# Kernel optimization log

Hardware: AMD Instinct MI355X
Metric: run time of the kernel (lower is better)

## Reference

```python
import jax, jax.numpy as jnp
import numpy as np

NS, NV = 32, 8                      # scalar / vector multiplicities (32x0e + 8x1o)
N_NODES, N_EDGES = 16384, 131072
NEF, HID = 128, 128                 # edge feature dim, MLP hidden
WN = NS*NS + NV*NS + NS*NV + NV*NV  # 1600 tensor-product weights per edge
D = NS + 3*NV                       # 56 node feature dim
INV_SQRT3 = 1.0/np.sqrt(3.0)        # CG coeff for 1o x 1o -> 0e
PATH_NORM = 1.0/np.sqrt(NS + NV)    # fan-in normalization per output irrep
EPS = 1e-5


def setup_inputs() -> dict:
    key = jax.random.key(0)
    ks = jax.random.split(key, 10)
    node_attr = jax.random.normal(ks[0], (N_NODES, D), jnp.float32)
    edge_index = jax.random.randint(ks[1], (2, N_EDGES), 0, N_NODES, dtype=jnp.int64)
    edge_attr = jax.random.normal(ks[2], (N_EDGES, NEF), jnp.float32)
    edge_sh = jax.random.normal(ks[3], (N_EDGES, 4), jnp.float32)
    W1 = jax.random.normal(ks[4], (NEF, HID), jnp.float32) / np.sqrt(NEF)
    b1 = jnp.zeros((HID,), jnp.float32)
    W2 = jax.random.normal(ks[5], (HID, WN), jnp.float32) / np.sqrt(HID)
    b2 = jnp.zeros((WN,), jnp.float32)
    bn_gamma = jnp.ones((NS + NV,), jnp.float32)   # per-irrep scale (scalars then vectors)
    bn_beta = jnp.zeros((NS,), jnp.float32)        # bias only on scalar irreps
    return dict(node_attr=node_attr, edge_attr=edge_attr, edge_sh=edge_sh,
                W1=W1, b1=b1, W2=W2, b2=b2, bn_gamma=bn_gamma, bn_beta=bn_beta,
                edge_index=edge_index)


def reference(node_attr, edge_attr, edge_sh, W1, b1, W2, b2, bn_gamma, bn_beta, edge_index):
    edge_src, edge_dst = edge_index[0], edge_index[1]

    # per-edge tensor-product weights from edge MLP (dropout=0, eval mode)
    w = jax.nn.relu(edge_attr @ W1 + b1) @ W2 + b2            # [E, WN]
    o0 = NS*NS; o1 = o0 + NV*NS; o2 = o1 + NS*NV
    w_ss = w[:, :o0].reshape(-1, NS, NS)   # 0e x 0e -> 0e
    w_vs = w[:, o0:o1].reshape(-1, NV, NS) # 1o x 1o -> 0e
    w_sv = w[:, o1:o2].reshape(-1, NS, NV) # 0e x 1o -> 1o
    w_vv = w[:, o2:].reshape(-1, NV, NV)   # 1o x 0e -> 1o

    # gather node features onto edges
    x = node_attr[edge_dst]                # [E, D]
    xs = x[:, :NS]                         # [E, NS]
    xv = x[:, NS:].reshape(-1, NV, 3)      # [E, NV, 3]
    ss = edge_sh[:, 0]                     # [E]
    sv = edge_sh[:, 1:4]                   # [E, 3]

    # CG tensor product with per-edge fully-connected weights
    dot_vv = jnp.einsum('eim,em->ei', xv, sv) * INV_SQRT3
    out_s = (jnp.einsum('eij,ei->ej', w_ss, xs) * ss[:, None]
             + jnp.einsum('eij,ei->ej', w_vs, dot_vv)) * PATH_NORM          # [E, NS]
    out_v = (jnp.einsum('eij,ei->ej', w_sv, xs)[:, :, None] * sv[:, None, :]
             + jnp.einsum('eij,eim->ejm', w_vv, xv) * ss[:, None, None]) * PATH_NORM  # [E, NV, 3]
    tp = jnp.concatenate([out_s, out_v.reshape(-1, 3*NV)], axis=-1)         # [E, D]

    # scatter-mean to source nodes
    sums = jax.ops.segment_sum(tp, edge_src, num_segments=N_NODES)
    cnt = jax.ops.segment_sum(jnp.ones((tp.shape[0], 1), tp.dtype), edge_src,
                              num_segments=N_NODES)
    out = sums / jnp.maximum(cnt, 1.0)

    # residual (in/out irreps identical -> zero padding is a no-op)
    out = out + node_attr

    # equivariant batch norm (training-mode batch statistics)
    s = out[:, :NS]
    v = out[:, NS:].reshape(-1, NV, 3)
    s = (s - s.mean(0)) / jnp.sqrt(s.var(0) + EPS) * bn_gamma[:NS] + bn_beta
    vn2 = (v * v).sum(-1).mean(0)                               # [NV] mean squared norm
    v = v / jnp.sqrt(vn2 + EPS)[None, :, None] * bn_gamma[NS:][None, :, None]
    return jnp.concatenate([s, v.reshape(-1, 3*NV)], axis=-1)
```

## Files before the change

kernel.cpp:

```cpp
#include <hip/hip_runtime.h>

typedef short short8 __attribute__((ext_vector_type(8)));
typedef unsigned short us4 __attribute__((ext_vector_type(4)));
typedef float floatx4 __attribute__((ext_vector_type(4)));
typedef unsigned short u16;

#define NN 16384
#define NE 131072
#define NEF_ 128
#define DD 56
#define INV_SQRT3F 0.57735026918962576f
#define PATH_NORMF 0.15811388300841897f

__device__ __forceinline__ float bf2f(u16 u) {
    union { unsigned int i; float f; } v; v.i = ((unsigned int)u) << 16; return v.f;
}
__device__ __forceinline__ u16 f2bf(float f) {
    union { float f; unsigned int i; } v; v.f = f;
    unsigned int r = v.i + 0x7fffu + ((v.i >> 16) & 1u);
    return (u16)(r >> 16);
}

__global__ __launch_bounds__(256) void prep(const float* __restrict__ W1,
                                            const float* __restrict__ W2,
                                            u16* __restrict__ W1f,
                                            u16* __restrict__ W2f,
                                            const int* __restrict__ eidx,
                                            int* __restrict__ deg) {
    int b = blockIdx.x;
    if (b < 864) {
        int i = b * 256 + threadIdx.x;
        if (i < 16384) {
            int cc = i >> 13, kk = (i >> 11) & 3, cg = (i >> 9) & 3;
            int lane = (i >> 3) & 63, j = i & 7;
            int q = lane >> 4, m = lane & 15;
            W1f[i] = f2bf(W1[(kk * 32 + q * 8 + j) * 128 + cc * 64 + cg * 16 + m]);
        } else {
            int f = i - 16384;
            int c = f >> 13, kk = (f >> 11) & 3, cg = (f >> 9) & 3;
            int lane = (f >> 3) & 63, j = f & 7;
            int q = lane >> 4, m = lane & 15;
            W2f[f] = f2bf(W2[(kk * 32 + q * 8 + j) * 1600 + c * 64 + cg * 16 + m]);
        }
    } else {
        int e = (b - 864) * 256 + threadIdx.x;
        atomicAdd(&deg[eidx[e]], 1);
    }
}

__global__ __launch_bounds__(1024) void deg_scan(const int* __restrict__ deg,
                                                 int* __restrict__ row_start,
                                                 int* __restrict__ cursor) {
    __shared__ int part[1024];
    const int t = threadIdx.x;
    const int base = t * 16;
    int loc[16];
    int s = 0;
    #pragma unroll
    for (int i = 0; i < 16; i++) { loc[i] = s; s += deg[base + i]; }
    part[t] = s;
    __syncthreads();
    for (int off = 1; off < 1024; off <<= 1) {
        int v = (t >= off) ? part[t - off] : 0;
        __syncthreads();
        part[t] += v;
        __syncthreads();
    }
    int pre = (t == 0) ? 0 : part[t - 1];
    #pragma unroll
    for (int i = 0; i < 16; i++) {
        int v = pre + loc[i];
        row_start[base + i] = v;
        cursor[base + i] = v;
    }
    if (t == 1023) row_start[16384] = pre + s;
}

__global__ __launch_bounds__(256) void edge_scatter(const int* __restrict__ eidx,
                                                    int* __restrict__ cursor,
                                                    int* __restrict__ edge_order) {
    int e = blockIdx.x * 256 + threadIdx.x;
    int p = atomicAdd(&cursor[eidx[e]], 1);
    edge_order[p] = e;
}

__global__ __launch_bounds__(512, 4) void tpconv(
    const float* __restrict__ node_attr, const float* __restrict__ edge_attr,
    const float* __restrict__ edge_sh, const u16* __restrict__ W1f,
    const float* __restrict__ b1, const u16* __restrict__ W2f,
    const float* __restrict__ b2, const int* __restrict__ eidx,
    const int* __restrict__ edge_order,
    float* __restrict__ tp)
{
    __shared__ __align__(16) char smem[48896];
    __shared__ int sND[64];
    __shared__ float sSH[4 * 64];
    u16*   sA  = (u16*)smem;
    u16*   B2a = (u16*)(smem + 17408);
    u16*   B2b = (u16*)smem;
    u16*   sF  = (u16*)(smem + 33792);
    float* b2s = (float*)(smem + 42496);
    float* Ssc  = (float*)smem;
    float* Svec = (float*)(smem + 16896);

    const int t = threadIdx.x;
    const int lane = t & 63;
    const int wv = t >> 6;
    const int m = lane & 15;
    const int q = lane >> 4;
    const int cg = wv & 3;
    const int eh = wv >> 2;
    const int eb = eh * 32;
    const int p0 = blockIdx.x * 64;

    short8 pre[2];
    #pragma unroll
    for (int ii = 0; ii < 2; ii++)
        pre[ii] = *(const short8*)&W2f[ii * 4096 + t * 8];

    for (int i = t; i < 1600; i += 512) b2s[i] = b2[i];

    #pragma unroll
    for (int ii = 0; ii < 4; ii++) {
        int cid = t + 512 * ii;
        int r = cid >> 5, s = cid & 31;
        int e = edge_order[p0 + r];
        const float* src = &edge_attr[(size_t)e * NEF_ + s * 4];
        us4 o;
        o.x = f2bf(src[0]); o.y = f2bf(src[1]); o.z = f2bf(src[2]); o.w = f2bf(src[3]);
        *(us4*)&sA[r * 136 + s * 4] = o;
    }
    if (t < 64) {
        int e = edge_order[p0 + t];
        sND[t] = eidx[NE + e];
        const float* sh = edge_sh + (size_t)e * 4;
        float ss = sh[0], s0 = sh[1], s1 = sh[2], s2 = sh[3];
        sSH[0 * 64 + t] = ss; sSH[1 * 64 + t] = s0;
        sSH[2 * 64 + t] = s1; sSH[3 * 64 + t] = s2;
        sF[64 * 64 + t] = f2bf(ss);
        sF[65 * 64 + t] = f2bf(s0);
        sF[66 * 64 + t] = f2bf(s1);
        sF[67 * 64 + t] = f2bf(s2);
    }
    __syncthreads();

    const int nd = sND[lane];
    #pragma unroll
    for (int ii = 0; ii < 7; ii++) {
        int d = wv + 8 * ii;
        float v = node_attr[(size_t)nd * DD + d];
        int row = (d < 32) ? d : (40 + d - 32);
        sF[row * 64 + lane] = f2bf(v);
    }
    {
        float x0 = node_attr[(size_t)nd * DD + 32 + 3 * wv + 0];
        float x1 = node_attr[(size_t)nd * DD + 32 + 3 * wv + 1];
        float x2 = node_attr[(size_t)nd * DD + 32 + 3 * wv + 2];
        float d = (x0 * sSH[1 * 64 + lane] + x1 * sSH[2 * 64 + lane]
                 + x2 * sSH[3 * 64 + lane]) * INV_SQRT3F;
        sF[(32 + wv) * 64 + lane] = f2bf(d);
    }
    __syncthreads();

    floatx4 hacc[2][2];
    #pragma unroll
    for (int cc = 0; cc < 2; cc++) {
        #pragma unroll
        for (int ii = 0; ii < 2; ii++)
            *(short8*)&B2a[ii * 4096 + t * 8] =
                *(const short8*)&W1f[cc * 8192 + ii * 4096 + t * 8];
        __syncthreads();
        {
            float bv = b1[cc * 64 + cg * 16 + m];
            hacc[cc][0] = (floatx4){bv, bv, bv, bv};
            hacc[cc][1] = hacc[cc][0];
        }
        #pragma unroll
        for (int kk = 0; kk < 4; kk++) {
            short8 a0 = *(const short8*)&sA[(eb      + m) * 136 + kk * 32 + q * 8];
            short8 a1 = *(const short8*)&sA[(eb + 16 + m) * 136 + kk * 32 + q * 8];
            short8 bA = *(const short8*)&B2a[(kk * 4 + cg) * 512 + lane * 8];
            hacc[cc][0] = __builtin_amdgcn_mfma_f32_16x16x32_bf16(a0, bA, hacc[cc][0], 0, 0, 0);
            hacc[cc][1] = __builtin_amdgcn_mfma_f32_16x16x32_bf16(a1, bA, hacc[cc][1], 0, 0, 0);
        }
        __syncthreads();
    }
    #pragma unroll
    for (int cc = 0; cc < 2; cc++)
      #pragma unroll
      for (int rt = 0; rt < 2; rt++)
        #pragma unroll
        for (int r = 0; r < 4; r++) {
            int e   = eb + rt * 16 + q * 4 + r;
            int col = cc * 64 + cg * 16 + m;
            float v = hacc[cc][rt][r];
            sA[e * 136 + col] = f2bf(v > 0.f ? v : 0.f);
        }
    __syncthreads();

    short8 hc[2][4];
    #pragma unroll
    for (int et = 0; et < 2; et++)
        #pragma unroll
        for (int kk = 0; kk < 4; kk++)
            hc[et][kk] = *(const short8*)&sA[(eb + et * 16 + m) * 136 + kk * 32 + q * 8];

    float ssc[2], svc[2][3];
    #pragma unroll
    for (int et = 0; et < 2; et++) {
        ssc[et] = bf2f(sF[64 * 64 + eb + et * 16 + m]);
        svc[et][0] = bf2f(sF[65 * 64 + eb + et * 16 + m]);
        svc[et][1] = bf2f(sF[66 * 64 + eb + et * 16 + m]);
        svc[et][2] = bf2f(sF[67 * 64 + eb + et * 16 + m]);
    }

    #pragma unroll
    for (int ii = 0; ii < 2; ii++)
        *(short8*)&B2a[ii * 4096 + t * 8] = pre[ii];
    #pragma unroll
    for (int ii = 0; ii < 2; ii++)
        pre[ii] = *(const short8*)&W2f[8192 + ii * 4096 + t * 8];
    __syncthreads();

    float tps[2][4];
    float tpv[2][4][3];
    #pragma unroll
    for (int et = 0; et < 2; et++)
        #pragma unroll
        for (int r = 0; r < 4; r++) {
            tps[et][r] = 0.f;
            tpv[et][r][0] = 0.f; tpv[et][r][1] = 0.f; tpv[et][r][2] = 0.f;
        }

    for (int c = 0; c < 25; c++) {
        const u16* rb = (c & 1) ? B2b : B2a;
        u16*       wb = (c & 1) ? B2a : B2b;

        floatx4 bias = *(const floatx4*)&b2s[c * 64 + cg * 16 + q * 4];
        floatx4 acc[2];
        acc[0] = bias; acc[1] = bias;
        #pragma unroll
        for (int kk = 0; kk < 4; kk++) {
            short8 a = *(const short8*)&rb[(kk * 4 + cg) * 512 + lane * 8];
            acc[0] = __builtin_amdgcn_mfma_f32_16x16x32_bf16(a, hc[0][kk], acc[0], 0, 0, 0);
            acc[1] = __builtin_amdgcn_mfma_f32_16x16x32_bf16(a, hc[1][kk], acc[1], 0, 0, 0);
        }

        if (c < 24) {
            #pragma unroll
            for (int ii = 0; ii < 2; ii++)
                *(short8*)&wb[ii * 4096 + t * 8] = pre[ii];
            if (c < 23) {
                #pragma unroll
                for (int ii = 0; ii < 2; ii++)
                    pre[ii] = *(const short8*)&W2f[(size_t)(c + 2) * 8192 + ii * 4096 + t * 8];
            }
        }

        if (c < 16) {
            const int i = 2 * c + (cg >> 1);
            #pragma unroll
            for (int et = 0; et < 2; et++) {
                float f = bf2f(sF[i * 64 + eb + et * 16 + m]) * ssc[et];
                #pragma unroll
                for (int r = 0; r < 4; r++) tps[et][r] += acc[et][r] * f;
            }
        } else if (c < 20) {
            const int i = 2 * (c - 16) + (cg >> 1);
            #pragma unroll
            for (int et = 0; et < 2; et++) {
                float f = bf2f(sF[(32 + i) * 64 + eb + et * 16 + m]);
                #pragma unroll
                for (int r = 0; r < 4; r++) tps[et][r] += acc[et][r] * f;
            }
        } else if (c < 24) {
            const int i = 8 * (c - 20) + cg * 2 + (q >> 1);
            #pragma unroll
            for (int et = 0; et < 2; et++) {
                float f = bf2f(sF[i * 64 + eb + et * 16 + m]);
                #pragma unroll
                for (int r = 0; r < 4; r++) {
                    float t0 = acc[et][r] * f;
                    tpv[et][r][0] += t0 * svc[et][0];
                    tpv[et][r][1] += t0 * svc[et][1];
                    tpv[et][r][2] += t0 * svc[et][2];
                }
            }
        } else {
            const int i = cg * 2 + (q >> 1);
            #pragma unroll
            for (int et = 0; et < 2; et++) {
                float x0 = bf2f(sF[(40 + 3 * i + 0) * 64 + eb + et * 16 + m]) * ssc[et];
                float x1 = bf2f(sF[(40 + 3 * i + 1) * 64 + eb + et * 16 + m]) * ssc[et];
                float x2 = bf2f(sF[(40 + 3 * i + 2) * 64 + eb + et * 16 + m]) * ssc[et];
                #pragma unroll
                for (int r = 0; r < 4; r++) {
                    tpv[et][r][0] += acc[et][r] * x0;
                    tpv[et][r][1] += acc[et][r] * x1;
                    tpv[et][r][2] += acc[et][r] * x2;
                }
            }
        }

        __syncthreads();
    }

    #pragma unroll
    for (int et = 0; et < 2; et++)
        #pragma unroll
        for (int r = 0; r < 4; r++)
            Ssc[(cg >> 1) * 2112 + (eb + et * 16 + m) * 33 + (cg & 1) * 16 + q * 4 + r] = tps[et][r];
    #pragma unroll
    for (int et = 0; et < 2; et++)
        #pragma unroll
        for (int r = 0; r < 4; r++)
            #pragma unroll
            for (int mm = 0; mm < 3; mm++) {
                float v = tpv[et][r][mm];
                v += __shfl_xor(v, 32, 64);
                if (q < 2)
                    Svec[cg * 1600 + (eb + et * 16 + m) * 25 + ((q & 1) * 4 + r) * 3 + mm] = v;
            }
    __syncthreads();

    for (int idx = t; idx < 3584; idx += 512) {
        int e = idx / 56, d = idx - e * 56;
        float v;
        if (d < 32) {
            v = Ssc[e * 33 + d] + Ssc[2112 + e * 33 + d];
        } else {
            int dd = d - 32;
            v = Svec[e * 25 + dd] + Svec[1600 + e * 25 + dd]
              + Svec[3200 + e * 25 + dd] + Svec[4800 + e * 25 + dd];
        }
        tp[(size_t)(p0 + e) * DD + d] = v * PATH_NORMF;
    }
}

__global__ __launch_bounds__(256) void gather_finalize(
    const float* __restrict__ tp, const int* __restrict__ row_start,
    const float* __restrict__ node_attr,
    float* __restrict__ ybuf, float* __restrict__ partial)
{
    __shared__ float ps[4][72];
    const int wv = threadIdx.x >> 6, lane = threadIdx.x & 63;
    const int n = blockIdx.x * 4 + wv;
    const int beg = row_start[n], end = row_start[n + 1];
    if (lane < 56) {
        float acc = 0.f;
        for (int p = beg; p < end; p++)
            acc += tp[(size_t)p * DD + lane];
        float inv = 1.f / fmaxf((float)(end - beg), 1.f);
        float y = acc * inv + node_attr[(size_t)n * DD + lane];
        ybuf[(size_t)n * DD + lane] = y;
        if (lane < 32) {
            ps[wv][lane] = y;
            ps[wv][32 + lane] = y * y;
        } else {
            float vv = y * y;
            float v1 = __shfl_down(vv, 1, 64);
            float v2 = __shfl_down(vv, 2, 64);
            int l3 = lane - 32;
            if (l3 % 3 == 0) ps[wv][64 + l3 / 3] = vv + v1 + v2;
        }
    }
    __syncthreads();
    const int t = threadIdx.x;
    if (t < 72)
        partial[(size_t)blockIdx.x * 72 + t] = ps[0][t] + ps[1][t] + ps[2][t] + ps[3][t];
}

__global__ __launch_bounds__(256) void bn_reduce(const float* __restrict__ partial,
                                                 float* __restrict__ stats)
{
    __shared__ float red[256];
    const int d = blockIdx.x;
    const int t = threadIdx.x;
    float a = 0.f;
    for (int i = t; i < 4096; i += 256) a += partial[(size_t)i * 72 + d];
    red[t] = a;
    __syncthreads();
    for (int off = 128; off > 0; off >>= 1) {
        if (t < off) red[t] += red[t + off];
        __syncthreads();
    }
    if (t == 0) stats[d] = red[0] * (1.f / 16384.f);
}

__global__ __launch_bounds__(256) void bn_apply(
    const float* __restrict__ ybuf, const float* __restrict__ stats,
    const float* __restrict__ gamma, const float* __restrict__ beta,
    float* __restrict__ out)
{
    const int i = blockIdx.x * 256 + threadIdx.x;
    const int n = i / 56;
    const int d = i - n * 56;
    float y = ybuf[i];
    float o;
    if (d < 32) {
        float mn  = stats[d];
        float var = stats[32 + d] - mn * mn;
        o = (y - mn) * rsqrtf(var + 1e-5f) * gamma[d] + beta[d];
    } else {
        int jv = (d - 32) / 3;
        o = y * rsqrtf(stats[64 + jv] + 1e-5f) * gamma[32 + jv];
    }
    out[i] = o;
}

extern "C" void kernel_launch(void* const* d_in, const int* in_sizes, int n_in,
                              void* d_out, int out_size, void* d_ws, size_t ws_size,
                              hipStream_t stream)
{
    const float* node_attr = (const float*)d_in[0];
    const float* edge_attr = (const float*)d_in[1];
    const float* edge_sh   = (const float*)d_in[2];
    const float* W1        = (const float*)d_in[3];
    const float* b1        = (const float*)d_in[4];
    const float* W2        = (const float*)d_in[5];
    const float* b2        = (const float*)d_in[6];
    const float* gamma     = (const float*)d_in[7];
    const float* beta      = (const float*)d_in[8];
    const int*   eidx      = (const int*)d_in[9];

    char* ws = (char*)d_ws;
    u16*   W1f        = (u16*)(ws);
    u16*   W2f        = (u16*)(ws + 32768);
    int*   deg        = (int*)(ws + 442368);
    int*   row_start  = (int*)(ws + 507904);
    int*   cursor     = (int*)(ws + 573696);
    int*   edge_order = (int*)(ws + 639232);
    float* stats      = (float*)(ws + 1163520);
    float* partial    = (float*)(ws + 1164032);
    float* tp         = (float*)(ws + 2343680);
    float* ybuf       = (float*)(ws + 31703808);

    (void)hipMemsetAsync(deg, 0, 65536, stream);
    hipLaunchKernelGGL(prep,            dim3(1376), dim3(256),  0, stream,
                       W1, W2, W1f, W2f, eidx, deg);
    hipLaunchKernelGGL(deg_scan,        dim3(1),    dim3(1024), 0, stream, deg, row_start, cursor);
    hipLaunchKernelGGL(edge_scatter,    dim3(512),  dim3(256),  0, stream, eidx, cursor, edge_order);
    hipLaunchKernelGGL(tpconv,          dim3(2048), dim3(512),  0, stream,
                       node_attr, edge_attr, edge_sh, W1f, b1, W2f, b2, eidx, edge_order, tp);
    hipLaunchKernelGGL(gather_finalize, dim3(4096), dim3(256),  0, stream,
                       tp, row_start, node_attr, ybuf, partial);
    hipLaunchKernelGGL(bn_reduce,       dim3(72),   dim3(256),  0, stream, partial, stats);
    hipLaunchKernelGGL(bn_apply,        dim3(3584), dim3(256),  0, stream,
                       ybuf, stats, gamma, beta, (float*)d_out);
}
```

Before: 252.5 us.

## Fuse gather, BN reduce and BN apply into one cooperative kernel

Replaces the three tail kernels (gather_finalize, bn_reduce, bn_apply) with one cooperative launch of 1024 blocks that uses grid-wide syncs between phases. Each block now handles 16 nodes and keeps per-thread running sums, so there are fewer partial rows for the reduction. This removes two kernel launches and their gaps, in exchange for two grid barriers and lower parallelism in the gather phase. The ybuf round trip through memory is still there.

```diff
diff --git a/kernel.cpp b/kernel.cpp
--- a/kernel.cpp
+++ b/kernel.cpp
@@ -1,4 +1,5 @@
 #include <hip/hip_runtime.h>
+#include <hip/hip_cooperative_groups.h>
 
 typedef short short8 __attribute__((ext_vector_type(8)));
 typedef unsigned short us4 __attribute__((ext_vector_type(4)));
@@ -337,75 +338,84 @@
     }
 }
 
-__global__ __launch_bounds__(256) void gather_finalize(
+__global__ __launch_bounds__(256) void tail_fused(
     const float* __restrict__ tp, const int* __restrict__ row_start,
     const float* __restrict__ node_attr,
-    float* __restrict__ ybuf, float* __restrict__ partial)
+    const float* __restrict__ gamma, const float* __restrict__ beta,
+    float* __restrict__ ybuf, float* __restrict__ partial,
+    float* __restrict__ stats, float* __restrict__ out)
 {
+    cooperative_groups::grid_group grid = cooperative_groups::this_grid();
     __shared__ float ps[4][72];
-    const int wv = threadIdx.x >> 6, lane = threadIdx.x & 63;
-    const int n = blockIdx.x * 4 + wv;
-    const int beg = row_start[n], end = row_start[n + 1];
-    if (lane < 56) {
-        float acc = 0.f;
-        for (int p = beg; p < end; p++)
-            acc += tp[(size_t)p * DD + lane];
-        float inv = 1.f / fmaxf((float)(end - beg), 1.f);
-        float y = acc * inv + node_attr[(size_t)n * DD + lane];
-        ybuf[(size_t)n * DD + lane] = y;
-        if (lane < 32) {
-            ps[wv][lane] = y;
-            ps[wv][32 + lane] = y * y;
-        } else {
-            float vv = y * y;
-            float v1 = __shfl_down(vv, 1, 64);
-            float v2 = __shfl_down(vv, 2, 64);
-            int l3 = lane - 32;
-            if (l3 % 3 == 0) ps[wv][64 + l3 / 3] = vv + v1 + v2;
-        }
-    }
-    __syncthreads();
+    __shared__ float red[256];
     const int t = threadIdx.x;
+    const int wv = t >> 6, lane = t & 63;
+
+    float ysum = 0.f, y2sum = 0.f, vacc = 0.f;
+    const int l3 = lane - 32;
+    #pragma unroll 1
+    for (int s = 0; s < 4; s++) {
+        const int n = blockIdx.x * 16 + wv * 4 + s;
+        const int beg = row_start[n], end = row_start[n + 1];
+        if (lane < 56) {
+            float acc = 0.f;
+            for (int p = beg; p < end; p++)
+                acc += tp[(size_t)p * DD + lane];
+            float inv = 1.f / fmaxf((float)(end - beg), 1.f);
+            float y = acc * inv + node_attr[(size_t)n * DD + lane];
+            ybuf[(size_t)n * DD + lane] = y;
+            if (lane < 32) {
+                ysum += y; y2sum += y * y;
+            } else {
+                float vv = y * y;
+                float v1 = __shfl_down(vv, 1, 64);
+                float v2 = __shfl_down(vv, 2, 64);
+                if (l3 % 3 == 0) vacc += vv + v1 + v2;
+            }
+        }
+    }
+    if (lane < 32) {
+        ps[wv][lane] = ysum;
+        ps[wv][32 + lane] = y2sum;
+    } else if (lane < 56 && l3 % 3 == 0) {
+        ps[wv][64 + l3 / 3] = vacc;
+    }
+    __syncthreads();
     if (t < 72)
         partial[(size_t)blockIdx.x * 72 + t] = ps[0][t] + ps[1][t] + ps[2][t] + ps[3][t];
-}
-
-__global__ __launch_bounds__(256) void bn_reduce(const float* __restrict__ partial,
-                                                 float* __restrict__ stats)
-{
-    __shared__ float red[256];
-    const int d = blockIdx.x;
-    const int t = threadIdx.x;
-    float a = 0.f;
-    for (int i = t; i < 4096; i += 256) a += partial[(size_t)i * 72 + d];
-    red[t] = a;
-    __syncthreads();
-    for (int off = 128; off > 0; off >>= 1) {
-        if (t < off) red[t] += red[t + off];
-        __syncthreads();
-    }
-    if (t == 0) stats[d] = red[0] * (1.f / 16384.f);
-}
-
-__global__ __launch_bounds__(256) void bn_apply(
-    const float* __restrict__ ybuf, const float* __restrict__ stats,
-    const float* __restrict__ gamma, const float* __restrict__ beta,
-    float* __restrict__ out)
-{
-    const int i = blockIdx.x * 256 + threadIdx.x;
-    const int n = i / 56;
-    const int d = i - n * 56;
-    float y = ybuf[i];
-    float o;
-    if (d < 32) {
-        float mn  = stats[d];
-        float var = stats[32 + d] - mn * mn;
-        o = (y - mn) * rsqrtf(var + 1e-5f) * gamma[d] + beta[d];
-    } else {
-        int jv = (d - 32) / 3;
-        o = y * rsqrtf(stats[64 + jv] + 1e-5f) * gamma[32 + jv];
-    }
-    out[i] = o;
+
+    grid.sync();
+
+    if (blockIdx.x < 72) {
+        const int d = blockIdx.x;
+        float a = 0.f;
+        for (int i = t; i < 1024; i += 256) a += partial[(size_t)i * 72 + d];
+        red[t] = a;
+        __syncthreads();
+        for (int off = 128; off > 0; off >>= 1) {
+            if (t < off) red[t] += red[t + off];
+            __syncthreads();
+        }
+        if (t == 0) stats[d] = red[0] * (1.f / 16384.f);
+    }
+
+    grid.sync();
+
+    for (int i = blockIdx.x * 256 + t; i < 917504; i += 262144) {
+        int n = i / 56;
+        int d = i - n * 56;
+        float y = ybuf[i];
+        float o;
+        if (d < 32) {
+            float mn  = stats[d];
+            float var = stats[32 + d] - mn * mn;
+            o = (y - mn) * rsqrtf(var + 1e-5f) * gamma[d] + beta[d];
+        } else {
+            int jv = (d - 32) / 3;
+            o = y * rsqrtf(stats[64 + jv] + 1e-5f) * gamma[32 + jv];
+        }
+        out[i] = o;
+    }
 }
 
 extern "C" void kernel_launch(void* const* d_in, const int* in_sizes, int n_in,
@@ -436,15 +446,18 @@
     float* ybuf       = (float*)(ws + 31703808);
 
     (void)hipMemsetAsync(deg, 0, 65536, stream);
-    hipLaunchKernelGGL(prep,            dim3(1376), dim3(256),  0, stream,
+    hipLaunchKernelGGL(prep,         dim3(1376), dim3(256),  0, stream,
                        W1, W2, W1f, W2f, eidx, deg);
-    hipLaunchKernelGGL(deg_scan,        dim3(1),    dim3(1024), 0, stream, deg, row_start, cursor);
-    hipLaunchKernelGGL(edge_scatter,    dim3(512),  dim3(256),  0, stream, eidx, cursor, edge_order);
-    hipLaunchKernelGGL(tpconv,          dim3(2048), dim3(512),  0, stream,
+    hipLaunchKernelGGL(deg_scan,     dim3(1),    dim3(1024), 0, stream, deg, row_start, cursor);
+    hipLaunchKernelGGL(edge_scatter, dim3(512),  dim3(256),  0, stream, eidx, cursor, edge_order);
+    hipLaunchKernelGGL(tpconv,       dim3(2048), dim3(512),  0, stream,
                        node_attr, edge_attr, edge_sh, W1f, b1, W2f, b2, eidx, edge_order, tp);
-    hipLaunchKernelGGL(gather_finalize, dim3(4096), dim3(256),  0, stream,
-                       tp, row_start, node_attr, ybuf, partial);
-    hipLaunchKernelGGL(bn_reduce,       dim3(72),   dim3(256),  0, stream, partial, stats);
-    hipLaunchKernelGGL(bn_apply,        dim3(3584), dim3(256),  0, stream,
-                       ybuf, stats, gamma, beta, (float*)d_out);
-}
+    {
+        float* outp = (float*)d_out;
+        void* args[] = { (void*)&tp, (void*)&row_start, (void*)&node_attr,
+                         (void*)&gamma, (void*)&beta,
+                         (void*)&ybuf, (void*)&partial, (void*)&stats, (void*)&outp };
+        (void)hipLaunchCooperativeKernel((const void*)tail_fused, dim3(1024), dim3(256),
+                                         args, 0, stream);
+    }
+}
```

New measurement: 489.1 us. 1.94x slower.
